# Kernel tuning notes

Measured on AMD Instinct MI355X. Metric: run time of the kernel, lower is better.

The kernel has to match this reference:

```python
import jax, jax.numpy as jnp
import numpy as np

N_NODES = 50000
N_EDGES = 800000
N_PAIRS = 200000
IN_DIM = 128
HID = 64
OUT_DIM = 1


def _gat_layer(x, W, a_l, a_r, src, dst, n_nodes):
    # Single-head GAT (DGL-style): z = xW; attention logits from learned
    # left/right vectors; softmax over incoming edges of each dst node.
    z = x @ W                                   # [N, H]
    el = z @ a_l                                # [N]
    er = z @ a_r                                # [N]
    e = jax.nn.leaky_relu(el[src] + er[dst], 0.2)   # [E]
    emax = jax.ops.segment_max(e, dst, num_segments=n_nodes)  # [N]
    ex = jnp.exp(e - emax[dst])                 # [E], stable softmax numerator
    denom = jax.ops.segment_sum(ex, dst, num_segments=n_nodes)  # [N]
    msg = ex[:, None] * z[src]                  # [E, H]
    agg = jax.ops.segment_sum(msg, dst, num_segments=n_nodes)   # [N, H]
    return agg / jnp.maximum(denom, 1e-9)[:, None]


def setup_inputs() -> dict:
    key = jax.random.key(0)
    ks = jax.random.split(key, 10)
    feat = jax.random.normal(ks[0], (N_NODES, IN_DIM), dtype=jnp.float32)
    src = jax.random.randint(ks[1], (N_EDGES,), 0, N_NODES, dtype=jnp.int32)
    dst = jax.random.randint(ks[2], (N_EDGES,), 0, N_NODES, dtype=jnp.int32)
    # query pairs: take existing edges so the has_edges_between mask is true
    pair_src = src[:N_PAIRS]
    pair_dst = dst[:N_PAIRS]
    s1 = 1.0 / np.sqrt(IN_DIM)
    s2 = 1.0 / np.sqrt(HID)
    W1 = jax.random.normal(ks[3], (IN_DIM, HID), dtype=jnp.float32) * s1
    al1 = jax.random.normal(ks[4], (HID,), dtype=jnp.float32) * s2
    ar1 = jax.random.normal(ks[5], (HID,), dtype=jnp.float32) * s2
    W2 = jax.random.normal(ks[6], (HID, HID), dtype=jnp.float32) * s2
    al2 = jax.random.normal(ks[7], (HID,), dtype=jnp.float32) * s2
    ar2 = jax.random.normal(ks[8], (HID,), dtype=jnp.float32) * s2
    Wc = jax.random.normal(ks[9], (2 * HID, OUT_DIM), dtype=jnp.float32) * s2
    bc = jnp.zeros((OUT_DIM,), dtype=jnp.float32)
    return {"feat": feat, "W1": W1, "al1": al1, "ar1": ar1,
            "W2": W2, "al2": al2, "ar2": ar2, "Wc": Wc, "bc": bc,
            "src": src, "dst": dst, "pair_src": pair_src, "pair_dst": pair_dst}


def reference(feat, W1, al1, ar1, W2, al2, ar2, Wc, bc, src, dst, pair_src, pair_dst):
    src = src.astype(jnp.int32)
    dst = dst.astype(jnp.int32)
    # two hetero GAT layers (single ntype -> mean aggregate is identity) + ReLU
    h = jax.nn.relu(_gat_layer(feat, W1, al1, ar1, src, dst, N_NODES))
    h = jax.nn.relu(_gat_layer(h, W2, al2, ar2, src, dst, N_NODES))
    # has_edges_between(pair_src, pair_dst): membership test via sorted edge keys
    ekeys = src.astype(jnp.int64) * N_NODES + dst.astype(jnp.int64)
    skeys = jnp.sort(ekeys)
    pkeys = pair_src.astype(jnp.int64) * N_NODES + pair_dst.astype(jnp.int64)
    idx = jnp.clip(jnp.searchsorted(skeys, pkeys), 0, N_EDGES - 1)
    mask = (skeys[idx] == pkeys)                 # [P] bool
    # gather endpoint embeddings, concat, classify, sigmoid; invalid rows -> 0
    hs = h[pair_src]                             # [P, H]
    hd = h[pair_dst]                             # [P, H]
    h_pair = jnp.concatenate([hs, hd], axis=1)   # [P, 2H]
    out = jax.nn.sigmoid(h_pair @ Wc + bc)       # [P, OUT]
    return out * mask[:, None].astype(out.dtype)
```

## Files before the change

### kernel.cpp

```cpp
#include <hip/hip_runtime.h>
#include <cstdint>

#define N_NODES 50000
#define N_EDGES 800000
#define N_PAIRS 200000
#define IN_DIM 128
#define HID 64
#define N_WAVES_GEMM (N_NODES / 16)
#define NB1 196
#define CHUNK ((N_EDGES + NB1 - 1) / NB1)
#define MHIST (NB1 * NB1)
#define SBG ((MHIST + 255) / 256)
#define MB_GEMM ((N_WAVES_GEMM + 3) / 4)
#define NODE_BLOCKS ((N_NODES + 3) / 4)
#define MEMBER_BLOCKS (N_PAIRS / 32)

typedef __attribute__((ext_vector_type(8))) short bf16x8;
typedef __attribute__((ext_vector_type(4))) float f32x4;

__device__ __forceinline__ unsigned short bf16_rne(float f) {
    unsigned u = __float_as_uint(f);
    unsigned t = u + 0x7FFFu + ((u >> 16) & 1u);
    return (unsigned short)(t >> 16);
}
__device__ __forceinline__ void bf2f(unsigned u, float& a, float& b) {
    a = __uint_as_float(u << 16);
    b = __uint_as_float(u & 0xFFFF0000u);
}

__global__ __launch_bounds__(256) void hist_prep(
    const int* __restrict__ dst, int* __restrict__ histHi,
    const float* __restrict__ W1, const float* __restrict__ W2,
    unsigned short* __restrict__ w1hi, unsigned short* __restrict__ w1lo,
    unsigned short* __restrict__ w2hi, unsigned short* __restrict__ w2lo)
{
    const int t = threadIdx.x, b = blockIdx.x;
    if (b < NB1) {
        __shared__ int hist[256];
        hist[t] = 0; __syncthreads();
        const int beg = b * CHUNK, end = min(beg + CHUNK, N_EDGES);
        for (int e = beg + t; e < end; e += 256) atomicAdd(&hist[dst[e] >> 8], 1);
        __syncthreads();
        if (t < NB1) histHi[t * NB1 + b] = hist[t];
    } else {
        int tid = (b - NB1) * 256 + t;
        if (tid < 8192) {
            int jj = tid & 7, lane = (tid >> 3) & 63, tt = (tid >> 9) & 3, ks = tid >> 11;
            int k = ks * 32 + (lane >> 4) * 8 + jj;
            int n = tt * 16 + (lane & 15);
            float f = W1[k * HID + n];
            unsigned short hi = bf16_rne(f);
            float fhi = __uint_as_float(((unsigned)hi) << 16);
            w1hi[tid] = hi;
            w1lo[tid] = bf16_rne(f - fhi);
        }
        if (tid < 4096) {
            int jj = tid & 7, lane = (tid >> 3) & 63, tt = (tid >> 9) & 3, ks = tid >> 11;
            int k = ks * 32 + (lane >> 4) * 8 + jj;
            int n = tt * 16 + (lane & 15);
            float f = W2[k * HID + n];
            unsigned short hi = bf16_rne(f);
            float fhi = __uint_as_float(((unsigned)hi) << 16);
            w2hi[tid] = hi;
            w2lo[tid] = bf16_rne(f - fhi);
        }
    }
}

__global__ __launch_bounds__(256) void scan1g(
    int* __restrict__ histHi, int* __restrict__ bsums)
{
    __shared__ int sh[256];
    const int t = threadIdx.x;
    const int i = blockIdx.x * 256 + t;
    int v = (i < MHIST) ? histHi[i] : 0;
    sh[t] = v; __syncthreads();
    #pragma unroll
    for (int off = 1; off < 256; off <<= 1) {
        int x = sh[t];
        int a = (t >= off) ? sh[t - off] : 0;
        __syncthreads();
        sh[t] = x + a;
        __syncthreads();
    }
    if (i < MHIST) histHi[i] = sh[t] - v;
    if (t == 255) bsums[blockIdx.x] = sh[255];
}

__device__ __forceinline__ void scan_bsums(const int* __restrict__ bsums,
                                           int* sh, int* exb, int t)
{
    int v = (t < SBG) ? bsums[t] : 0;
    sh[t] = v; __syncthreads();
    #pragma unroll
    for (int off = 1; off < 256; off <<= 1) {
        int x = sh[t];
        int a = (t >= off) ? sh[t - off] : 0;
        __syncthreads();
        sh[t] = x + a;
        __syncthreads();
    }
    exb[t] = sh[t] - v;
    __syncthreads();
}

__device__ __forceinline__ void gemm1_body(
    int wave, int lane,
    const float* __restrict__ x,
    const unsigned short* __restrict__ whi, const unsigned short* __restrict__ wlo,
    const float* __restrict__ al, const float* __restrict__ ar,
    unsigned short* __restrict__ z, float* __restrict__ el, float* __restrict__ er)
{
    const int i0 = wave * 16;
    const int m = lane & 15, quad = lane >> 4;
    f32x4 acc[4] = {{0.f,0.f,0.f,0.f},{0.f,0.f,0.f,0.f},{0.f,0.f,0.f,0.f},{0.f,0.f,0.f,0.f}};
    const float* xrow = x + (size_t)(i0 + m) * IN_DIM;

    #pragma unroll 1
    for (int ks = 0; ks < 4; ++ks) {
        const float4 xv0 = *(const float4*)&xrow[ks * 32 + quad * 8];
        const float4 xv1 = *(const float4*)&xrow[ks * 32 + quad * 8 + 4];
        float xs[8] = {xv0.x, xv0.y, xv0.z, xv0.w, xv1.x, xv1.y, xv1.z, xv1.w};
        bf16x8 ahi, alo;
        #pragma unroll
        for (int jj = 0; jj < 8; ++jj) {
            unsigned short hb = bf16_rne(xs[jj]);
            float fhi = __uint_as_float(((unsigned)hb) << 16);
            ahi[jj] = (short)hb;
            alo[jj] = (short)bf16_rne(xs[jj] - fhi);
        }
        #pragma unroll
        for (int t = 0; t < 4; ++t) {
            const bf16x8 bhi = *(const bf16x8*)&whi[(((ks * 4 + t) * 64) + lane) * 8];
            const bf16x8 blo = *(const bf16x8*)&wlo[(((ks * 4 + t) * 64) + lane) * 8];
            acc[t] = __builtin_amdgcn_mfma_f32_16x16x32_bf16(ahi, bhi, acc[t], 0, 0, 0);
            acc[t] = __builtin_amdgcn_mfma_f32_16x16x32_bf16(ahi, blo, acc[t], 0, 0, 0);
            acc[t] = __builtin_amdgcn_mfma_f32_16x16x32_bf16(alo, bhi, acc[t], 0, 0, 0);
        }
    }
    #pragma unroll
    for (int r = 0; r < 4; ++r) {
        const int row = quad * 4 + r;
        float se = 0.f, sr = 0.f;
        #pragma unroll
        for (int t = 0; t < 4; ++t) {
            float v = acc[t][r];
            z[(size_t)(i0 + row) * HID + t * 16 + m] = bf16_rne(v);
            se = fmaf(v, al[t * 16 + m], se);
            sr = fmaf(v, ar[t * 16 + m], sr);
        }
        #pragma unroll
        for (int off = 1; off < 16; off <<= 1) {
            se += __shfl_xor(se, off, 64);
            sr += __shfl_xor(sr, off, 64);
        }
        if (m == 0) { el[i0 + row] = se; er[i0 + row] = sr; }
    }
}

__global__ __launch_bounds__(256) void scatter_gemm1(
    const int* __restrict__ src, const int* __restrict__ dst,
    const int* __restrict__ histEx, const int* __restrict__ bsums,
    unsigned* __restrict__ pairs,
    const float* __restrict__ x,
    const unsigned short* __restrict__ whi, const unsigned short* __restrict__ wlo,
    const float* __restrict__ al, const float* __restrict__ ar,
    unsigned short* __restrict__ z, float* __restrict__ el, float* __restrict__ er)
{
    const int b = blockIdx.x;
    if (b < NB1) {
        __shared__ int sh[256], exb[256], base[256];
        const int t = threadIdx.y * 64 + threadIdx.x;
        scan_bsums(bsums, sh, exb, t);
        if (t < NB1) {
            int idx = t * NB1 + b;
            base[t] = histEx[idx] + exb[idx >> 8];
        }
        __syncthreads();
        const int beg = b * CHUNK, end = min(beg + CHUNK, N_EDGES);
        for (int e = beg + t; e < end; e += 256) {
            int s = src[e], d = dst[e];
            int pos = atomicAdd(&base[d >> 8], 1);
            pairs[pos] = ((unsigned)s << 16) | (unsigned)d;
        }
    } else {
        const int wave = (b - NB1) * 4 + threadIdx.y;
        if (wave < N_WAVES_GEMM)
            gemm1_body(wave, threadIdx.x, x, whi, wlo, al, ar, z, el, er);
    }
}

__global__ __launch_bounds__(256) void seg_sort(
    const unsigned* __restrict__ pairs, const int* __restrict__ histEx,
    const int* __restrict__ bsums,
    int* __restrict__ row_start, unsigned short* __restrict__ csr_src)
{
    __shared__ int sh[256], exb[256], hist[256], sc[256], offs[256];
    const int t = threadIdx.x, b = blockIdx.x;
    scan_bsums(bsums, sh, exb, t);
    const int i0 = b * NB1;
    const int segStart = histEx[i0] + exb[i0 >> 8];
    int segEnd = N_EDGES;
    if (b < NB1 - 1) {
        const int i1 = (b + 1) * NB1;
        segEnd = histEx[i1] + exb[i1 >> 8];
    }
    hist[t] = 0; __syncthreads();
    for (int i = segStart + t; i < segEnd; i += 256)
        atomicAdd(&hist[pairs[i] & 255], 1);
    __syncthreads();
    int v = hist[t]; sc[t] = v; __syncthreads();
    #pragma unroll
    for (int off = 1; off < 256; off <<= 1) {
        int x = sc[t];
        int a = (t >= off) ? sc[t - off] : 0;
        __syncthreads();
        sc[t] = x + a;
        __syncthreads();
    }
    const int excl = sc[t] - v;
    offs[t] = segStart + excl;
    const int node = b * 256 + t;
    if (node <= N_NODES) row_start[node] = segStart + excl;
    __syncthreads();
    for (int i = segStart + t; i < segEnd; i += 256) {
        unsigned p = pairs[i];
        int pos = atomicAdd(&offs[p & 255], 1);
        csr_src[pos] = (unsigned short)(p >> 16);
    }
}

template <bool LAST>
__device__ __forceinline__ void agg_body(
    int i, int lane,
    const int* __restrict__ row_start, const unsigned short* __restrict__ csr_src,
    const float* __restrict__ el, const float* __restrict__ er,
    const unsigned short* __restrict__ z, unsigned short* __restrict__ hdst,
    const float* __restrict__ Wc, float* __restrict__ as, float* __restrict__ ad)
{
    const int rb = row_start[i], re = row_start[i + 1];
    const float er_i = er[i];
    const int es = lane >> 3;
    const int fl = lane & 7;

    float acc[8] = {0.f,0.f,0.f,0.f,0.f,0.f,0.f,0.f};
    float den = 0.f;

    int eA = rb + es;        bool vA = eA < re;
    int eB = eA + 8;         bool vB = eB < re;
    int sA = vA ? (int)csr_src[eA] : 0;
    int sB = vB ? (int)csr_src[eB] : 0;
    float elA = el[sA];
    uint4 zA = ((const uint4*)(z + (size_t)sA * HID))[fl];

    for (int e0 = rb; e0 < re; e0 += 8) {
        const int eC = e0 + 16 + es;
        const bool vC = eC < re;
        const int sC = vC ? (int)csr_src[eC] : 0;
        const float elB = el[sB];
        const uint4 zB = ((const uint4*)(z + (size_t)sB * HID))[fl];

        float x = elA + er_i;
        float lr = x > 0.f ? x : 0.2f * x;
        float ex = vA ? __expf(lr) : 0.f;
        float z0, z1, z2, z3, z4, z5, z6, z7;
        bf2f(zA.x, z0, z1); bf2f(zA.y, z2, z3);
        bf2f(zA.z, z4, z5); bf2f(zA.w, z6, z7);
        acc[0] = fmaf(ex, z0, acc[0]); acc[1] = fmaf(ex, z1, acc[1]);
        acc[2] = fmaf(ex, z2, acc[2]); acc[3] = fmaf(ex, z3, acc[3]);
        acc[4] = fmaf(ex, z4, acc[4]); acc[5] = fmaf(ex, z5, acc[5]);
        acc[6] = fmaf(ex, z6, acc[6]); acc[7] = fmaf(ex, z7, acc[7]);
        den += ex;

        sA = sB; vA = vB; elA = elB; zA = zB;
        sB = sC; vB = vC;
    }
    #pragma unroll
    for (int off = 8; off < 64; off <<= 1) {
        #pragma unroll
        for (int q = 0; q < 8; ++q) acc[q] += __shfl_xor(acc[q], off, 64);
        den += __shfl_xor(den, off, 64);
    }
    if (es == 0) {
        float inv = 1.f / fmaxf(den, 1e-9f);
        float hv[8];
        #pragma unroll
        for (int q = 0; q < 8; ++q) hv[q] = fmaxf(acc[q] * inv, 0.f);
        if (LAST) {
            float ps = 0.f, pd = 0.f;
            #pragma unroll
            for (int q = 0; q < 8; ++q) {
                ps = fmaf(hv[q], Wc[fl * 8 + q], ps);
                pd = fmaf(hv[q], Wc[HID + fl * 8 + q], pd);
            }
            #pragma unroll
            for (int off = 1; off < 8; off <<= 1) {
                ps += __shfl_xor(ps, off, 64);
                pd += __shfl_xor(pd, off, 64);
            }
            if (fl == 0) { as[i] = ps; ad[i] = pd; }
        } else {
            unsigned short o[8];
            #pragma unroll
            for (int q = 0; q < 8; ++q) o[q] = bf16_rne(hv[q]);
            uint4 pk;
            pk.x = (unsigned)o[0] | ((unsigned)o[1] << 16);
            pk.y = (unsigned)o[2] | ((unsigned)o[3] << 16);
            pk.z = (unsigned)o[4] | ((unsigned)o[5] << 16);
            pk.w = (unsigned)o[6] | ((unsigned)o[7] << 16);
            ((uint4*)hdst)[fl] = pk;
        }
    }
}

__global__ __launch_bounds__(256) void agg1_gemm2_member(
    const int* __restrict__ row_start, const unsigned short* __restrict__ csr_src,
    const float* __restrict__ el1, const float* __restrict__ er1,
    const unsigned short* __restrict__ z1,
    const unsigned short* __restrict__ whi, const unsigned short* __restrict__ wlo,
    const float* __restrict__ al, const float* __restrict__ ar,
    unsigned short* __restrict__ z2, float* __restrict__ el2, float* __restrict__ er2,
    const int* __restrict__ ps, const int* __restrict__ pd, int* __restrict__ found)
{
    const int b = blockIdx.x, lane = threadIdx.x, ty = threadIdx.y;
    if (b < N_WAVES_GEMM) {
        __shared__ __align__(16) unsigned short ht[16][72];
        const int i0 = b * 16;
        #pragma unroll 1
        for (int c = 0; c < 4; ++c) {
            const int r = ty * 4 + c;
            agg_body<false>(i0 + r, lane, row_start, csr_src, el1, er1, z1,
                            &ht[r][0], nullptr, nullptr, nullptr);
        }
        __syncthreads();
        if (ty == 0) {
            const int m = lane & 15, quad = lane >> 4;
            f32x4 acc[4] = {{0.f,0.f,0.f,0.f},{0.f,0.f,0.f,0.f},
                            {0.f,0.f,0.f,0.f},{0.f,0.f,0.f,0.f}};
            const unsigned short* xrow = &ht[m][0];
            #pragma unroll 1
            for (int ks = 0; ks < 2; ++ks) {
                const bf16x8 aa = *(const bf16x8*)&xrow[ks * 32 + quad * 8];
                #pragma unroll
                for (int tt = 0; tt < 4; ++tt) {
                    const bf16x8 bhi = *(const bf16x8*)&whi[(((ks * 4 + tt) * 64) + lane) * 8];
                    const bf16x8 blo = *(const bf16x8*)&wlo[(((ks * 4 + tt) * 64) + lane) * 8];
                    acc[tt] = __builtin_amdgcn_mfma_f32_16x16x32_bf16(aa, bhi, acc[tt], 0, 0, 0);
                    acc[tt] = __builtin_amdgcn_mfma_f32_16x16x32_bf16(aa, blo, acc[tt], 0, 0, 0);
                }
            }
            #pragma unroll
            for (int r = 0; r < 4; ++r) {
                const int row = quad * 4 + r;
                float se = 0.f, sr = 0.f;
                #pragma unroll
                for (int tt = 0; tt < 4; ++tt) {
                    float v = acc[tt][r];
                    z2[(size_t)(i0 + row) * HID + tt * 16 + m] = bf16_rne(v);
                    se = fmaf(v, al[tt * 16 + m], se);
                    sr = fmaf(v, ar[tt * 16 + m], sr);
                }
                #pragma unroll
                for (int off = 1; off < 16; off <<= 1) {
                    se += __shfl_xor(se, off, 64);
                    sr += __shfl_xor(sr, off, 64);
                }
                if (m == 0) { el2[i0 + row] = se; er2[i0 + row] = sr; }
            }
        }
    } else {
        const int r8 = lane & 7, g = lane >> 3;
        const int p = (b - N_WAVES_GEMM) * 32 + ty * 8 + g;
        const int s = ps[p], d = pd[p];
        const int rb = row_start[d], re = row_start[d + 1];
        int f = 0;
        for (int e = rb + r8; e < re; e += 8) f |= ((int)csr_src[e] == s) ? 1 : 0;
        #pragma unroll
        for (int off = 1; off < 8; off <<= 1) f |= __shfl_xor(f, off, 64);
        if (r8 == 0) found[p] = f;
    }
}

__global__ __launch_bounds__(256) void agg2(
    const int* __restrict__ row_start, const unsigned short* __restrict__ csr_src,
    const float* __restrict__ el, const float* __restrict__ er,
    const unsigned short* __restrict__ z, const float* __restrict__ Wc,
    float* __restrict__ as, float* __restrict__ ad)
{
    const int i = blockIdx.x * 4 + threadIdx.y;
    if (i < N_NODES)
        agg_body<true>(i, threadIdx.x, row_start, csr_src, el, er, z,
                       nullptr, Wc, as, ad);
}

__global__ __launch_bounds__(256) void pair_tiny(
    const int* __restrict__ ps, const int* __restrict__ pd,
    const float* __restrict__ as, const float* __restrict__ ad,
    const float* __restrict__ bc, const int* __restrict__ found,
    float* __restrict__ out)
{
    const int p = blockIdx.x * 256 + threadIdx.x;
    if (p >= N_PAIRS) return;
    float v = as[ps[p]] + ad[pd[p]] + bc[0];
    float sg = 1.f / (1.f + __expf(-v));
    out[p] = found[p] ? sg : 0.f;
}

extern "C" void kernel_launch(void* const* d_in, const int* in_sizes, int n_in,
                              void* d_out, int out_size, void* d_ws, size_t ws_size,
                              hipStream_t stream)
{
    const float* feat = (const float*)d_in[0];
    const float* W1   = (const float*)d_in[1];
    const float* al1  = (const float*)d_in[2];
    const float* ar1  = (const float*)d_in[3];
    const float* W2   = (const float*)d_in[4];
    const float* al2  = (const float*)d_in[5];
    const float* ar2  = (const float*)d_in[6];
    const float* Wc   = (const float*)d_in[7];
    const float* bc   = (const float*)d_in[8];
    const int* src    = (const int*)d_in[9];
    const int* dst    = (const int*)d_in[10];
    const int* psrc   = (const int*)d_in[11];
    const int* pdst   = (const int*)d_in[12];
    float* out = (float*)d_out;

    char* ws = (char*)d_ws;
    unsigned short* z  = (unsigned short*)ws;  ws += (size_t)N_NODES * HID * 2;
    unsigned short* z2 = (unsigned short*)ws;  ws += (size_t)N_NODES * HID * 2;
    float* el = (float*)ws;               ws += (size_t)N_NODES * 4;
    float* er = (float*)ws;               ws += (size_t)N_NODES * 4;
    float* as = (float*)ws;               ws += (size_t)N_NODES * 4;
    float* ad = (float*)ws;               ws += (size_t)N_NODES * 4;
    float* el2 = (float*)ws;              ws += (size_t)N_NODES * 4;
    float* er2 = (float*)ws;              ws += (size_t)N_NODES * 4;
    int* row_start = (int*)ws;            ws += (size_t)(N_NODES + 1) * 4;
    int* histHi = (int*)ws;               ws += (size_t)MHIST * 4;
    int* bsumsA = (int*)ws;               ws += (size_t)(SBG + 1) * 4;
    int* found = (int*)ws;                ws += (size_t)N_PAIRS * 4;
    ws = (char*)(((uintptr_t)ws + 255) & ~(uintptr_t)255);
    unsigned* pairs = (unsigned*)ws;      ws += (size_t)N_EDGES * 4;
    unsigned short* csr_src = (unsigned short*)ws;  ws += (size_t)N_EDGES * 2;
    ws = (char*)(((uintptr_t)ws + 255) & ~(uintptr_t)255);
    unsigned short* w1hi = (unsigned short*)ws;  ws += 8192 * 2;
    unsigned short* w1lo = (unsigned short*)ws;  ws += 8192 * 2;
    unsigned short* w2hi = (unsigned short*)ws;  ws += 4096 * 2;
    unsigned short* w2lo = (unsigned short*)ws;  ws += 4096 * 2;

    dim3 b64x4(64, 4);

    hist_prep<<<NB1 + 32, 256, 0, stream>>>(dst, histHi, W1, W2, w1hi, w1lo, w2hi, w2lo);
    scan1g<<<SBG, 256, 0, stream>>>(histHi, bsumsA);
    scatter_gemm1<<<NB1 + MB_GEMM, b64x4, 0, stream>>>(src, dst, histHi, bsumsA, pairs,
        feat, w1hi, w1lo, al1, ar1, z, el, er);
    seg_sort<<<NB1, 256, 0, stream>>>(pairs, histHi, bsumsA, row_start, csr_src);
    agg1_gemm2_member<<<N_WAVES_GEMM + MEMBER_BLOCKS, b64x4, 0, stream>>>(
        row_start, csr_src, el, er, z, w2hi, w2lo, al2, ar2,
        z2, el2, er2, psrc, pdst, found);
    agg2<<<NODE_BLOCKS, b64x4, 0, stream>>>(row_start, csr_src, el2, er2, z2, Wc, as, ad);
    pair_tiny<<<(N_PAIRS + 255) / 256, 256, 0, stream>>>(psrc, pdst, as, ad, bc, found, out);
}
```

Before: 185.2 us.

## Build CSR by per-node degree counting and global atomics instead of two-pass radix sort

Replaces the two-level radix sort (a coarse histogram by dst>>8, a scatter into pairs, then a segmented sort) with a direct counting sort. Per-node degrees are computed with global atomics, prefix-scanned, and edges are then scattered straight into csr_src using per-node atomic counters. This drops the seg_sort kernel, the intermediate pairs buffer and one pass over the edges. In exchange it adds a memset and heavy contention-free but uncoalesced global atomics. Edge order within each row is no longer deterministic, so floating-point summation order can vary between runs.

Measured after the change: 240.9 us. +30.1%, slower.

```diff
diff --git a/kernel.cpp b/kernel.cpp
--- a/kernel.cpp
+++ b/kernel.cpp
@@ -7,10 +7,10 @@
 #define IN_DIM 128
 #define HID 64
 #define N_WAVES_GEMM (N_NODES / 16)
-#define NB1 196
-#define CHUNK ((N_EDGES + NB1 - 1) / NB1)
-#define MHIST (NB1 * NB1)
-#define SBG ((MHIST + 255) / 256)
+#define NBS 196
+#define DEG_N (NBS * 256)
+#define EB 784
+#define EPB ((N_EDGES + EB - 1) / EB)
 #define MB_GEMM ((N_WAVES_GEMM + 3) / 4)
 #define NODE_BLOCKS ((N_NODES + 3) / 4)
 #define MEMBER_BLOCKS (N_PAIRS / 32)
@@ -29,21 +29,17 @@
 }
 
 __global__ __launch_bounds__(256) void hist_prep(
-    const int* __restrict__ dst, int* __restrict__ histHi,
+    const int* __restrict__ dst, int* __restrict__ deg,
     const float* __restrict__ W1, const float* __restrict__ W2,
     unsigned short* __restrict__ w1hi, unsigned short* __restrict__ w1lo,
     unsigned short* __restrict__ w2hi, unsigned short* __restrict__ w2lo)
 {
     const int t = threadIdx.x, b = blockIdx.x;
-    if (b < NB1) {
-        __shared__ int hist[256];
-        hist[t] = 0; __syncthreads();
-        const int beg = b * CHUNK, end = min(beg + CHUNK, N_EDGES);
-        for (int e = beg + t; e < end; e += 256) atomicAdd(&hist[dst[e] >> 8], 1);
-        __syncthreads();
-        if (t < NB1) histHi[t * NB1 + b] = hist[t];
+    if (b < EB) {
+        const int beg = b * EPB, end = min(beg + EPB, N_EDGES);
+        for (int e = beg + t; e < end; e += 256) atomicAdd(&deg[dst[e]], 1);
     } else {
-        int tid = (b - NB1) * 256 + t;
+        int tid = (b - EB) * 256 + t;
         if (tid < 8192) {
             int jj = tid & 7, lane = (tid >> 3) & 63, tt = (tid >> 9) & 3, ks = tid >> 11;
             int k = ks * 32 + (lane >> 4) * 8 + jj;
@@ -67,13 +63,13 @@
     }
 }
 
-__global__ __launch_bounds__(256) void scan1g(
-    int* __restrict__ histHi, int* __restrict__ bsums)
+__global__ __launch_bounds__(256) void scan_deg(
+    const int* __restrict__ deg, int* __restrict__ partial, int* __restrict__ bsums)
 {
     __shared__ int sh[256];
     const int t = threadIdx.x;
     const int i = blockIdx.x * 256 + t;
-    int v = (i < MHIST) ? histHi[i] : 0;
+    int v = deg[i];
     sh[t] = v; __syncthreads();
     #pragma unroll
     for (int off = 1; off < 256; off <<= 1) {
@@ -83,14 +79,14 @@
         sh[t] = x + a;
         __syncthreads();
     }
-    if (i < MHIST) histHi[i] = sh[t] - v;
+    partial[i] = sh[t] - v;
     if (t == 255) bsums[blockIdx.x] = sh[255];
 }
 
-__device__ __forceinline__ void scan_bsums(const int* __restrict__ bsums,
-                                           int* sh, int* exb, int t)
-{
-    int v = (t < SBG) ? bsums[t] : 0;
+__device__ __forceinline__ void scan_bsums_n(const int* __restrict__ bsums,
+                                             int* sh, int* exb, int t)
+{
+    int v = (t < NBS) ? bsums[t] : 0;
     sh[t] = v; __syncthreads();
     #pragma unroll
     for (int off = 1; off < 256; off <<= 1) {
@@ -160,73 +156,33 @@
 
 __global__ __launch_bounds__(256) void scatter_gemm1(
     const int* __restrict__ src, const int* __restrict__ dst,
-    const int* __restrict__ histEx, const int* __restrict__ bsums,
-    unsigned* __restrict__ pairs,
+    const int* __restrict__ partial, const int* __restrict__ bsums,
+    int* __restrict__ cnt, int* __restrict__ row_start,
+    unsigned short* __restrict__ csr_src,
     const float* __restrict__ x,
     const unsigned short* __restrict__ whi, const unsigned short* __restrict__ wlo,
     const float* __restrict__ al, const float* __restrict__ ar,
     unsigned short* __restrict__ z, float* __restrict__ el, float* __restrict__ er)
 {
     const int b = blockIdx.x;
-    if (b < NB1) {
-        __shared__ int sh[256], exb[256], base[256];
+    if (b < EB) {
+        __shared__ int sh[256], exb[256];
         const int t = threadIdx.y * 64 + threadIdx.x;
-        scan_bsums(bsums, sh, exb, t);
-        if (t < NB1) {
-            int idx = t * NB1 + b;
-            base[t] = histEx[idx] + exb[idx >> 8];
-        }
-        __syncthreads();
-        const int beg = b * CHUNK, end = min(beg + CHUNK, N_EDGES);
+        scan_bsums_n(bsums, sh, exb, t);
+        if (b < NBS) {
+            const int node = b * 256 + t;
+            if (node <= N_NODES) row_start[node] = partial[node] + exb[b];
+        }
+        const int beg = b * EPB, end = min(beg + EPB, N_EDGES);
         for (int e = beg + t; e < end; e += 256) {
             int s = src[e], d = dst[e];
-            int pos = atomicAdd(&base[d >> 8], 1);
-            pairs[pos] = ((unsigned)s << 16) | (unsigned)d;
+            int pos = partial[d] + exb[d >> 8] + atomicAdd(&cnt[d], 1);
+            csr_src[pos] = (unsigned short)s;
         }
     } else {
-        const int wave = (b - NB1) * 4 + threadIdx.y;
+        const int wave = (b - EB) * 4 + threadIdx.y;
         if (wave < N_WAVES_GEMM)
             gemm1_body(wave, threadIdx.x, x, whi, wlo, al, ar, z, el, er);
-    }
-}
-
-__global__ __launch_bounds__(256) void seg_sort(
-    const unsigned* __restrict__ pairs, const int* __restrict__ histEx,
-    const int* __restrict__ bsums,
-    int* __restrict__ row_start, unsigned short* __restrict__ csr_src)
-{
-    __shared__ int sh[256], exb[256], hist[256], sc[256], offs[256];
-    const int t = threadIdx.x, b = blockIdx.x;
-    scan_bsums(bsums, sh, exb, t);
-    const int i0 = b * NB1;
-    const int segStart = histEx[i0] + exb[i0 >> 8];
-    int segEnd = N_EDGES;
-    if (b < NB1 - 1) {
-        const int i1 = (b + 1) * NB1;
-        segEnd = histEx[i1] + exb[i1 >> 8];
-    }
-    hist[t] = 0; __syncthreads();
-    for (int i = segStart + t; i < segEnd; i += 256)
-        atomicAdd(&hist[pairs[i] & 255], 1);
-    __syncthreads();
-    int v = hist[t]; sc[t] = v; __syncthreads();
-    #pragma unroll
-    for (int off = 1; off < 256; off <<= 1) {
-        int x = sc[t];
-        int a = (t >= off) ? sc[t - off] : 0;
-        __syncthreads();
-        sc[t] = x + a;
-        __syncthreads();
-    }
-    const int excl = sc[t] - v;
-    offs[t] = segStart + excl;
-    const int node = b * 256 + t;
-    if (node <= N_NODES) row_start[node] = segStart + excl;
-    __syncthreads();
-    for (int i = segStart + t; i < segEnd; i += 256) {
-        unsigned p = pairs[i];
-        int pos = atomicAdd(&offs[p & 255], 1);
-        csr_src[pos] = (unsigned short)(p >> 16);
     }
 }
 
@@ -435,11 +391,12 @@
     float* el2 = (float*)ws;              ws += (size_t)N_NODES * 4;
     float* er2 = (float*)ws;              ws += (size_t)N_NODES * 4;
     int* row_start = (int*)ws;            ws += (size_t)(N_NODES + 1) * 4;
-    int* histHi = (int*)ws;               ws += (size_t)MHIST * 4;
-    int* bsumsA = (int*)ws;               ws += (size_t)(SBG + 1) * 4;
+    int* deg = (int*)ws;                  ws += (size_t)DEG_N * 4;
+    int* cnt = (int*)ws;                  ws += (size_t)DEG_N * 4;
+    int* partial = (int*)ws;              ws += (size_t)DEG_N * 4;
+    int* bsums = (int*)ws;                ws += 256 * 4;
     int* found = (int*)ws;                ws += (size_t)N_PAIRS * 4;
     ws = (char*)(((uintptr_t)ws + 255) & ~(uintptr_t)255);
-    unsigned* pairs = (unsigned*)ws;      ws += (size_t)N_EDGES * 4;
     unsigned short* csr_src = (unsigned short*)ws;  ws += (size_t)N_EDGES * 2;
     ws = (char*)(((uintptr_t)ws + 255) & ~(uintptr_t)255);
     unsigned short* w1hi = (unsigned short*)ws;  ws += 8192 * 2;
@@ -449,11 +406,11 @@
 
     dim3 b64x4(64, 4);
 
-    hist_prep<<<NB1 + 32, 256, 0, stream>>>(dst, histHi, W1, W2, w1hi, w1lo, w2hi, w2lo);
-    scan1g<<<SBG, 256, 0, stream>>>(histHi, bsumsA);
-    scatter_gemm1<<<NB1 + MB_GEMM, b64x4, 0, stream>>>(src, dst, histHi, bsumsA, pairs,
-        feat, w1hi, w1lo, al1, ar1, z, el, er);
-    seg_sort<<<NB1, 256, 0, stream>>>(pairs, histHi, bsumsA, row_start, csr_src);
+    hipMemsetAsync(deg, 0, (size_t)2 * DEG_N * 4, stream);
+    hist_prep<<<EB + 32, 256, 0, stream>>>(dst, deg, W1, W2, w1hi, w1lo, w2hi, w2lo);
+    scan_deg<<<NBS, 256, 0, stream>>>(deg, partial, bsums);
+    scatter_gemm1<<<EB + MB_GEMM, b64x4, 0, stream>>>(src, dst, partial, bsums,
+        cnt, row_start, csr_src, feat, w1hi, w1lo, al1, ar1, z, el, er);
     agg1_gemm2_member<<<N_WAVES_GEMM + MEMBER_BLOCKS, b64x4, 0, stream>>>(
         row_start, csr_src, el, er, z, w2hi, w2lo, al2, ar2,
         z2, el2, er2, psrc, pdst, found);
```
